# Kernel tuning notes

Measured on AMD Instinct MI355X. Metric: run time of the kernel, lower is better.

The kernel has to match this reference:

```python
import jax, jax.numpy as jnp
import numpy as np

N, E, G, H, NF, EF, GF, L = 204800, 600000, 3200, 128, 16, 5, 8, 6
EPS = 1e-5


def setup_inputs() -> dict:
    key = jax.random.key(0)
    ks = jax.random.split(key, 24)
    s = 0.05
    inp = {
        'x': jax.random.normal(ks[0], (N, NF), jnp.float32),
        'edge_index': jax.random.randint(ks[1], (2, E), 0, N, jnp.int32),
        'edge_attr': jax.random.normal(ks[2], (E, EF), jnp.float32),
        'global_features': jax.random.normal(ks[3], (G, GF), jnp.float32),
        'batch': (jnp.arange(N, dtype=jnp.int32) // (N // G)),
        'node_w': jax.random.normal(ks[4], (NF, H), jnp.float32) * s,
        'node_b': jnp.zeros((H,), jnp.float32),
        'edge_w': jax.random.normal(ks[5], (EF, H), jnp.float32) * s,
        'edge_b': jnp.zeros((H,), jnp.float32),
        'rel_w': jax.random.normal(ks[6], (L, H, H), jnp.float32) * s,
        'rel_b': jnp.zeros((L, H), jnp.float32),
        'root_w': jax.random.normal(ks[7], (L, H, H), jnp.float32) * s,
        'bn_gamma': jnp.ones((L, H), jnp.float32),
        'bn_beta': jnp.zeros((L, H), jnp.float32),
        'gate_w1': jax.random.normal(ks[8], (H, H), jnp.float32) * s,
        'gate_b1': jnp.zeros((H,), jnp.float32),
        'gate_w2': jax.random.normal(ks[9], (H, 1), jnp.float32) * s,
        'gate_b2': jnp.zeros((1,), jnp.float32),
        'gf_w': jax.random.normal(ks[10], (GF, H), jnp.float32) * s,
        'gf_b': jnp.zeros((H,), jnp.float32),
        'gi_w': jax.random.normal(ks[11], (2 * H, H), jnp.float32) * s,
        'gi_b': jnp.zeros((H,), jnp.float32),
    }
    return inp


def reference(x, edge_index, edge_attr, global_features, batch,
              node_w, node_b, edge_w, edge_b,
              rel_w, rel_b, root_w, bn_gamma, bn_beta,
              gate_w1, gate_b1, gate_w2, gate_b2,
              gf_w, gf_b, gi_w, gi_b):
    n = x.shape[0]
    src, dst = edge_index[0], edge_index[1]
    h = x @ node_w + node_b                       # [N,H]
    ea = edge_attr @ edge_w + edge_b              # [E,H]
    for i in range(L):
        identity = h
        msg = h[src] * ea                         # [E,H] gather + edge weighting
        agg = jax.ops.segment_sum(msg, dst, num_segments=n)  # scatter-add
        h2 = agg @ rel_w[i] + rel_b[i] + h @ root_w[i]        # GraphConv
        mean = jnp.mean(h2, axis=0)
        var = jnp.mean(jnp.square(h2 - mean), axis=0)         # biased (BN train)
        h2 = (h2 - mean) * jax.lax.rsqrt(var + EPS) * bn_gamma[i] + bn_beta[i]
        h = jax.nn.relu(h2 + identity)
    # GlobalAttention: segment softmax over gate scores, weighted sum of h
    gate = (jax.nn.relu(h @ gate_w1 + gate_b1) @ gate_w2 + gate_b2)[:, 0]  # [N]
    m = jax.ops.segment_max(gate, batch, num_segments=G)
    e = jnp.exp(gate - m[batch])
    ssum = jax.ops.segment_sum(e, batch, num_segments=G)
    alpha = e / ssum[batch]
    pooled = jax.ops.segment_sum(alpha[:, None] * h, batch, num_segments=G)  # [G,H]
    gf = global_features @ gf_w + gf_b
    global_embedding = jnp.concatenate([pooled, gf], axis=1) @ gi_w + gi_b
    return (h, global_embedding)
```

## Files before the change

### kernel.cpp

```cpp
#include <hip/hip_runtime.h>
#include <math.h>

#define N_NODES 204800
#define N_EDGES 600000
#define N_GRAPH 3200
#define H 128
#define NF 16
#define EF 5
#define GF 8
#define LAYERS 6
#define SEG 64
#define EPSV 1e-5f
#define NB_SCAN 800
#define NBLK 3200

typedef __attribute__((ext_vector_type(8))) short bf16x8;
typedef __attribute__((ext_vector_type(4))) float f32x4;

__device__ inline float bf2f(unsigned int u) {
    return __builtin_bit_cast(float, u << 16);
}
__device__ inline unsigned short f2bf(float f) {
    unsigned int u = __builtin_bit_cast(unsigned int, f);
    u += 0x7fffu + ((u >> 16) & 1u);
    return (unsigned short)(u >> 16);
}
__device__ inline float uif(unsigned int u) { return __builtin_bit_cast(float, u); }

__global__ __launch_bounds__(64) void k_wpack_init(
    const float* __restrict__ nw, unsigned short* __restrict__ nwp)
{
    int nb = blockIdx.x;
    int l = threadIdx.x;
    int col = nb * 16 + (l & 15);
    int kb = (l >> 4) * 8;
    unsigned short tmp[8];
#pragma unroll
    for (int m = 0; m < 8; ++m) {
        int k = kb + m;
        tmp[m] = (k < NF) ? f2bf(nw[(size_t)k * H + col]) : (unsigned short)0;
    }
    *(uint4*)(nwp + ((size_t)nb * 64 + l) * 8) = *(uint4*)tmp;
}

__global__ __launch_bounds__(256) void k_init_mfma(
    const float* __restrict__ x, const unsigned short* __restrict__ nwp,
    const float* __restrict__ node_b, unsigned short* __restrict__ hb)
{
    __shared__ unsigned short xt[64][40];
    int tid = threadIdx.x;
    int w = tid >> 6, l = tid & 63;
    int n0 = blockIdx.x * 64;
    int lr = l & 15, hi = l >> 4;

    int row = tid >> 2, q = tid & 3;
    float4 xv = *(const float4*)(x + (size_t)(n0 + row) * NF + q * 4);
    xt[row][q * 4 + 0] = f2bf(xv.x);
    xt[row][q * 4 + 1] = f2bf(xv.y);
    xt[row][q * 4 + 2] = f2bf(xv.z);
    xt[row][q * 4 + 3] = f2bf(xv.w);
    *(uint2*)&xt[row][16 + q * 4] = make_uint2(0, 0);
    __syncthreads();

    f32x4 acc[4][2];
#pragma unroll
    for (int rb = 0; rb < 4; ++rb) {
        acc[rb][0] = (f32x4){0.f, 0.f, 0.f, 0.f};
        acc[rb][1] = (f32x4){0.f, 0.f, 0.f, 0.f};
    }
    const bf16x8* wv = (const bf16x8*)nwp;
    bf16x8 b0 = wv[(2 * w + 0) * 64 + l];
    bf16x8 b1 = wv[(2 * w + 1) * 64 + l];
#pragma unroll
    for (int rb = 0; rb < 4; ++rb) {
        bf16x8 a = *(const bf16x8*)&xt[rb * 16 + lr][hi * 8];
        acc[rb][0] = __builtin_amdgcn_mfma_f32_16x16x32_bf16(a, b0, acc[rb][0], 0, 0, 0);
        acc[rb][1] = __builtin_amdgcn_mfma_f32_16x16x32_bf16(a, b1, acc[rb][1], 0, 0, 0);
    }

#pragma unroll
    for (int nbl = 0; nbl < 2; ++nbl) {
        int col = w * 32 + nbl * 16 + lr;
        float bs = node_b[col];
#pragma unroll
        for (int rb = 0; rb < 4; ++rb)
#pragma unroll
            for (int jj = 0; jj < 4; ++jj)
                hb[(size_t)(n0 + rb * 16 + hi * 4 + jj) * H + col] = f2bf(acc[rb][nbl][jj] + bs);
    }
}

__global__ __launch_bounds__(64) void k_wpack(
    const float* __restrict__ relw, const float* __restrict__ rootw,
    unsigned short* __restrict__ wp)
{
    int bid = blockIdx.x;
    int i = bid >> 6, f = bid & 63;
    int nb = f >> 3, ks = f & 7;
    int l = threadIdx.x;
    const float* src = (ks < 4) ? (relw + (size_t)i * H * H) : (rootw + (size_t)i * H * H);
    int ksl = ks & 3;
    int col = nb * 16 + (l & 15);
    int kbase = ksl * 32 + (l >> 4) * 8;
    unsigned short tmp[8];
#pragma unroll
    for (int m = 0; m < 8; ++m)
        tmp[m] = f2bf(src[(size_t)(kbase + m) * H + col]);
    *(uint4*)(wp + ((size_t)bid * 64 + l) * 8) = *(uint4*)tmp;
}

__global__ __launch_bounds__(64) void k_wpack_gate(
    const float* __restrict__ gw1, unsigned short* __restrict__ gwp)
{
    int bid = blockIdx.x;
    int nb = bid >> 2, ks = bid & 3;
    int l = threadIdx.x;
    int col = nb * 16 + (l & 15);
    int kbase = ks * 32 + (l >> 4) * 8;
    unsigned short tmp[8];
#pragma unroll
    for (int m = 0; m < 8; ++m)
        tmp[m] = f2bf(gw1[(size_t)(kbase + m) * H + col]);
    *(uint4*)(gwp + ((size_t)bid * 64 + l) * 8) = *(uint4*)tmp;
}

__global__ __launch_bounds__(256) void k_deg(const int* __restrict__ ei, int* __restrict__ deg)
{
    int e = blockIdx.x * 256 + threadIdx.x;
    if (e < N_EDGES) atomicAdd(&deg[ei[N_EDGES + e]], 1);
}

__global__ __launch_bounds__(256) void k_scan1(
    const int* __restrict__ deg, int* __restrict__ rowtmp, int* __restrict__ bsum)
{
    __shared__ int sh[256];
    int t = threadIdx.x;
    int i = blockIdx.x * 256 + t;
    int v = deg[i];
    sh[t] = v;
    __syncthreads();
    for (int off = 1; off < 256; off <<= 1) {
        int a = (t >= off) ? sh[t - off] : 0;
        __syncthreads();
        sh[t] += a;
        __syncthreads();
    }
    rowtmp[i] = sh[t] - v;
    if (t == 255) bsum[blockIdx.x] = sh[255];
}

__global__ void k_scan2(int* __restrict__ bsum, int* __restrict__ boff)
{
    __shared__ int sh[256];
    __shared__ int carry;
    int t = threadIdx.x;
    if (t == 0) carry = 0;
    __syncthreads();
    for (int base = 0; base < NB_SCAN; base += 256) {
        int i = base + t;
        int v = (i < NB_SCAN) ? bsum[i] : 0;
        sh[t] = v;
        __syncthreads();
        for (int off = 1; off < 256; off <<= 1) {
            int a = (t >= off) ? sh[t - off] : 0;
            __syncthreads();
            sh[t] += a;
            __syncthreads();
        }
        if (i < NB_SCAN) boff[i] = carry + sh[t] - v;
        __syncthreads();
        if (t == 0) carry += sh[255];
        __syncthreads();
    }
}

__global__ __launch_bounds__(256) void k_scan3(
    const int* __restrict__ rowtmp, const int* __restrict__ boff,
    int* __restrict__ rowptr, int* __restrict__ cursor)
{
    int i = blockIdx.x * 256 + threadIdx.x;
    int r = rowtmp[i] + boff[blockIdx.x];
    rowptr[i] = r;
    cursor[i] = r;
    if (i == 0) rowptr[N_NODES] = N_EDGES;
}

__global__ __launch_bounds__(256) void k_scatter(
    const int* __restrict__ ei, const float* __restrict__ eattr,
    int* __restrict__ cursor, uint4* __restrict__ recs)
{
    int e = blockIdx.x * 256 + threadIdx.x;
    if (e >= N_EDGES) return;
    int d = ei[N_EDGES + e];
    const float* ar = eattr + (size_t)e * EF;
    float c0 = ar[0], c1 = ar[1], c2 = ar[2], c3 = ar[3], c4 = ar[4];
    int pos = atomicAdd(&cursor[d], 1);
    uint4 q0, q1;
    q0.x = (unsigned int)ei[e];
    q0.y = __builtin_bit_cast(unsigned int, c0);
    q0.z = __builtin_bit_cast(unsigned int, c1);
    q0.w = __builtin_bit_cast(unsigned int, c2);
    q1.x = __builtin_bit_cast(unsigned int, c3);
    q1.y = __builtin_bit_cast(unsigned int, c4);
    q1.z = 0; q1.w = 0;
    recs[2 * (size_t)pos]     = q0;
    recs[2 * (size_t)pos + 1] = q1;
}

#define FOLD(jj, q0, q1, hv)                                                   \
    if ((jj) < jend) {                                                         \
        while ((jj) >= nend) {                                                 \
            *(unsigned int*)(aggb + (size_t)(n0 + cur) * H + 2 * l) =          \
                (unsigned int)f2bf(a0) | ((unsigned int)f2bf(a1) << 16);       \
            a0 = 0.f; a1 = 0.f; ++cur; nend = __shfl(rpv, cur + 1);            \
        }                                                                      \
        float ea0 = eb2.x, ea1 = eb2.y;                                        \
        float c0 = uif((q0).y), c1 = uif((q0).z), c2 = uif((q0).w);            \
        float c3 = uif((q1).x), c4 = uif((q1).y);                              \
        ea0 += c0 * ew2[0].x + c1 * ew2[1].x + c2 * ew2[2].x + c3 * ew2[3].x + c4 * ew2[4].x; \
        ea1 += c0 * ew2[0].y + c1 * ew2[1].y + c2 * ew2[2].y + c3 * ew2[3].y + c4 * ew2[4].y; \
        a0 += bf2f((hv) & 0xffffu) * ea0;                                      \
        a1 += bf2f((hv) >> 16) * ea1;                                          \
    }

__global__ __launch_bounds__(256) void k_agg(
    const int* __restrict__ rowptr, const uint4* __restrict__ recs,
    const float* __restrict__ edge_w, const float* __restrict__ edge_b,
    const unsigned short* __restrict__ hb, unsigned short* __restrict__ aggb)
{
    int w = threadIdx.x >> 6, l = threadIdx.x & 63;
    int n0 = (blockIdx.x * 4 + w) * 8;
    float2 ew2[EF];
#pragma unroll
    for (int k = 0; k < EF; ++k) ew2[k] = ((const float2*)(edge_w + k * H))[l];
    float2 eb2 = ((const float2*)edge_b)[l];

    int rpv = rowptr[n0 + (l < 9 ? l : 8)];
    int jbeg = __shfl(rpv, 0), jend = __shfl(rpv, 8);
    int cur = 0;
    int nend = __shfl(rpv, 1);
    float a0 = 0.f, a1 = 0.f;

    for (int j = jbeg; j < jend; j += 4) {
        int jc1 = min(j + 1, jend - 1);
        int jc2 = min(j + 2, jend - 1);
        int jc3 = min(j + 3, jend - 1);
        uint4 qa0 = recs[2 * (size_t)j],   qa1 = recs[2 * (size_t)j + 1];
        uint4 qb0 = recs[2 * (size_t)jc1], qb1 = recs[2 * (size_t)jc1 + 1];
        uint4 qc0 = recs[2 * (size_t)jc2], qc1 = recs[2 * (size_t)jc2 + 1];
        uint4 qd0 = recs[2 * (size_t)jc3], qd1 = recs[2 * (size_t)jc3 + 1];
        unsigned int hva = *(const unsigned int*)(hb + (size_t)(int)qa0.x * H + 2 * l);
        unsigned int hvb = *(const unsigned int*)(hb + (size_t)(int)qb0.x * H + 2 * l);
        unsigned int hvc = *(const unsigned int*)(hb + (size_t)(int)qc0.x * H + 2 * l);
        unsigned int hvd = *(const unsigned int*)(hb + (size_t)(int)qd0.x * H + 2 * l);
        FOLD(j,     qa0, qa1, hva);
        FOLD(j + 1, qb0, qb1, hvb);
        FOLD(j + 2, qc0, qc1, hvc);
        FOLD(j + 3, qd0, qd1, hvd);
    }
    while (cur < 8) {
        *(unsigned int*)(aggb + (size_t)(n0 + cur) * H + 2 * l) =
            (unsigned int)f2bf(a0) | ((unsigned int)f2bf(a1) << 16);
        a0 = 0.f; a1 = 0.f; ++cur;
    }
}

__global__ __launch_bounds__(256) void k_gemm_mfma(
    const unsigned short* __restrict__ aggb,
    const unsigned short* __restrict__ hb,
    const unsigned short* __restrict__ wp,
    const float* __restrict__ relb,
    unsigned short* __restrict__ h2b,
    float* __restrict__ pbuf)
{
    __shared__ unsigned short smA[64 * 128];
    __shared__ unsigned short smH[64 * 128];
    int tid = threadIdx.x;
    int w = tid >> 6, l = tid & 63;
    int bid = blockIdx.x;
    int n0 = bid * 64;
    int lr = l & 15, hi = l >> 4;

    const char* aggp = (const char*)(aggb + (size_t)n0 * H);
    const char* hbp  = (const char*)(hb  + (size_t)n0 * H);
    char* sA = (char*)smA;
    char* sH = (char*)smH;
#pragma unroll
    for (int i = 0; i < 4; ++i) {
        int o = (i * 256 + tid) * 16;
        int row = o >> 8;
        int col = o & 255;
        int scol = col ^ ((row & 7) << 4);
        uint4 va = *(const uint4*)(aggp + o);
        uint4 vh = *(const uint4*)(hbp + o);
        *(uint4*)(sA + row * 256 + scol) = va;
        *(uint4*)(sH + row * 256 + scol) = vh;
    }
    __syncthreads();

    f32x4 acc[4][2];
#pragma unroll
    for (int rb = 0; rb < 4; ++rb) {
        acc[rb][0] = (f32x4){0.f, 0.f, 0.f, 0.f};
        acc[rb][1] = (f32x4){0.f, 0.f, 0.f, 0.f};
    }

    const bf16x8* wv = (const bf16x8*)wp;
#pragma unroll
    for (int ks = 0; ks < 4; ++ks) {
        bf16x8 b0 = wv[((2 * w + 0) * 8 + ks) * 64 + l];
        bf16x8 b1 = wv[((2 * w + 1) * 8 + ks) * 64 + l];
#pragma unroll
        for (int rb = 0; rb < 4; ++rb) {
            int r = rb * 16 + lr;
            int bc = (ks * 64 + hi * 16) ^ ((r & 7) << 4);
            bf16x8 a = *(const bf16x8*)(sA + r * 256 + bc);
            acc[rb][0] = __builtin_amdgcn_mfma_f32_16x16x32_bf16(a, b0, acc[rb][0], 0, 0, 0);
            acc[rb][1] = __builtin_amdgcn_mfma_f32_16x16x32_bf16(a, b1, acc[rb][1], 0, 0, 0);
        }
    }
#pragma unroll
    for (int ks = 0; ks < 4; ++ks) {
        bf16x8 b0 = wv[((2 * w + 0) * 8 + 4 + ks) * 64 + l];
        bf16x8 b1 = wv[((2 * w + 1) * 8 + 4 + ks) * 64 + l];
#pragma unroll
        for (int rb = 0; rb < 4; ++rb) {
            int r = rb * 16 + lr;
            int bc = (ks * 64 + hi * 16) ^ ((r & 7) << 4);
            bf16x8 a = *(const bf16x8*)(sH + r * 256 + bc);
            acc[rb][0] = __builtin_amdgcn_mfma_f32_16x16x32_bf16(a, b0, acc[rb][0], 0, 0, 0);
            acc[rb][1] = __builtin_amdgcn_mfma_f32_16x16x32_bf16(a, b1, acc[rb][1], 0, 0, 0);
        }
    }

#pragma unroll
    for (int nbl = 0; nbl < 2; ++nbl) {
        int col = w * 32 + nbl * 16 + lr;
        float bs = relb[col];
        float csum = 0.f, csq = 0.f;
#pragma unroll
        for (int rb = 0; rb < 4; ++rb) {
#pragma unroll
            for (int jj = 0; jj < 4; ++jj) {
                float v = acc[rb][nbl][jj] + bs;
                h2b[(size_t)(n0 + rb * 16 + hi * 4 + jj) * H + col] = f2bf(v);
                csum += v; csq += v * v;
            }
        }
        csum += __shfl_xor(csum, 16); csum += __shfl_xor(csum, 32);
        csq  += __shfl_xor(csq, 16);  csq  += __shfl_xor(csq, 32);
        if (hi == 0) {
            pbuf[(size_t)col * NBLK + bid]         = csum;
            pbuf[(size_t)(128 + col) * NBLK + bid] = csq;
        }
    }
}

__global__ __launch_bounds__(256) void k_red(
    const float* __restrict__ pbuf, const float* __restrict__ gamma,
    const float* __restrict__ beta, float* __restrict__ stats)
{
    __shared__ float sh[8];
    int c = blockIdx.x;
    int t = threadIdx.x;
    float s = 0.f, q = 0.f;
    const float* ps = pbuf + (size_t)c * NBLK;
    const float* pq = pbuf + (size_t)(128 + c) * NBLK;
    for (int i = t; i < NBLK; i += 256) { s += ps[i]; q += pq[i]; }
#pragma unroll
    for (int off = 32; off >= 1; off >>= 1) {
        s += __shfl_xor(s, off);
        q += __shfl_xor(q, off);
    }
    if ((t & 63) == 0) { sh[t >> 6] = s; sh[4 + (t >> 6)] = q; }
    __syncthreads();
    if (t == 0) {
        float S = sh[0] + sh[1] + sh[2] + sh[3];
        float Q = sh[4] + sh[5] + sh[6] + sh[7];
        float mean = S / (float)N_NODES;
        float var = fmaxf(Q / (float)N_NODES - mean * mean, 0.f);
        float scale = gamma[c] * rsqrtf(var + EPSV);
        stats[c] = scale;
        stats[128 + c] = beta[c] - mean * scale;
    }
}

template<bool LAST>
__global__ __launch_bounds__(256) void k_bn_apply(
    const unsigned short* __restrict__ h2b, const float* __restrict__ stats,
    unsigned short* __restrict__ hb, float* __restrict__ h)
{
    __shared__ float ssc[H], ssh[H];
    int tid = threadIdx.x;
    if (tid < H) {
        ssc[tid] = stats[tid];
        ssh[tid] = stats[128 + tid];
    }
    __syncthreads();
    size_t base = ((size_t)blockIdx.x * 256 + tid) * 8;
    int c = (int)(base & 127);
    uint4 hv2 = *(const uint4*)(h2b + base);
    uint4 hvp = *(const uint4*)(hb + base);
    unsigned int u2[4] = {hv2.x, hv2.y, hv2.z, hv2.w};
    unsigned int up[4] = {hvp.x, hvp.y, hvp.z, hvp.w};
    float o[8];
#pragma unroll
    for (int k = 0; k < 4; ++k) {
        float vlo = bf2f(u2[k] & 0xffffu), vhi = bf2f(u2[k] >> 16);
        float plo = bf2f(up[k] & 0xffffu), phi = bf2f(up[k] >> 16);
        o[2 * k]     = fmaxf(vlo * ssc[c + 2 * k]     + ssh[c + 2 * k]     + plo, 0.f);
        o[2 * k + 1] = fmaxf(vhi * ssc[c + 2 * k + 1] + ssh[c + 2 * k + 1] + phi, 0.f);
    }
    uint4 pk;
    pk.x = (unsigned int)f2bf(o[0]) | ((unsigned int)f2bf(o[1]) << 16);
    pk.y = (unsigned int)f2bf(o[2]) | ((unsigned int)f2bf(o[3]) << 16);
    pk.z = (unsigned int)f2bf(o[4]) | ((unsigned int)f2bf(o[5]) << 16);
    pk.w = (unsigned int)f2bf(o[6]) | ((unsigned int)f2bf(o[7]) << 16);
    *(uint4*)(hb + base) = pk;
    if (LAST) {
        *(float4*)(h + base)     = make_float4(o[0], o[1], o[2], o[3]);
        *(float4*)(h + base + 4) = make_float4(o[4], o[5], o[6], o[7]);
    }
}

__global__ __launch_bounds__(256) void k_gate_pool(
    const unsigned short* __restrict__ hb,
    const unsigned short* __restrict__ gwp,
    const float* __restrict__ b1, const float* __restrict__ w2,
    const float* __restrict__ b2, float* __restrict__ pooled)
{
    __shared__ float Red[512];
    __shared__ float al[64];
    int tid = threadIdx.x;
    int w = tid >> 6, l = tid & 63;
    int lr = l & 15, hi = l >> 4;
    int g = blockIdx.x;
    int n0 = g * SEG;

    f32x4 acc[4][2];
#pragma unroll
    for (int rb = 0; rb < 4; ++rb) {
        acc[rb][0] = (f32x4){0.f, 0.f, 0.f, 0.f};
        acc[rb][1] = (f32x4){0.f, 0.f, 0.f, 0.f};
    }
    const bf16x8* wv = (const bf16x8*)gwp;
#pragma unroll
    for (int ks = 0; ks < 4; ++ks) {
        bf16x8 bb0 = wv[((2 * w + 0) * 4 + ks) * 64 + l];
        bf16x8 bb1 = wv[((2 * w + 1) * 4 + ks) * 64 + l];
#pragma unroll
        for (int rb = 0; rb < 4; ++rb) {
            bf16x8 a = *(const bf16x8*)(hb + (size_t)(n0 + rb * 16 + lr) * H + ks * 32 + hi * 8);
            acc[rb][0] = __builtin_amdgcn_mfma_f32_16x16x32_bf16(a, bb0, acc[rb][0], 0, 0, 0);
            acc[rb][1] = __builtin_amdgcn_mfma_f32_16x16x32_bf16(a, bb1, acc[rb][1], 0, 0, 0);
        }
    }
    int col0 = w * 32 + lr, col1 = w * 32 + 16 + lr;
    float b10 = b1[col0], b11 = b1[col1];
    float w20 = w2[col0], w21 = w2[col1];
    float p[4][4];
#pragma unroll
    for (int rb = 0; rb < 4; ++rb)
#pragma unroll
        for (int jj = 0; jj < 4; ++jj) {
            float v0 = fmaxf(acc[rb][0][jj] + b10, 0.f);
            float v1 = fmaxf(acc[rb][1][jj] + b11, 0.f);
            float s = v0 * w20 + v1 * w21;
            s += __shfl_xor(s, 1); s += __shfl_xor(s, 2);
            s += __shfl_xor(s, 4); s += __shfl_xor(s, 8);
            p[rb][jj] = s;
        }
    if (lr == 0) {
#pragma unroll
        for (int rb = 0; rb < 4; ++rb)
#pragma unroll
            for (int jj = 0; jj < 4; ++jj)
                Red[w * 64 + rb * 16 + hi * 4 + jj] = p[rb][jj];
    }
    __syncthreads();
    if (tid < 64) {
        float gt = Red[tid] + Red[64 + tid] + Red[128 + tid] + Red[192 + tid] + b2[0];
        float m = gt;
#pragma unroll
        for (int off = 32; off >= 1; off >>= 1) m = fmaxf(m, __shfl_xor(m, off));
        float e = expf(gt - m);
        float s = e;
#pragma unroll
        for (int off = 32; off >= 1; off >>= 1) s += __shfl_xor(s, off);
        al[tid] = e / s;
    }
    __syncthreads();
    int cq = tid & 63, qd = tid >> 6;
    float p0 = 0.f, p1 = 0.f;
    const unsigned short* hbase = hb + (size_t)n0 * H;
    for (int j = qd * 16; j < qd * 16 + 16; ++j) {
        unsigned int hv = *(const unsigned int*)(hbase + (size_t)j * H + 2 * cq);
        float a = al[j];
        p0 += a * bf2f(hv & 0xffffu);
        p1 += a * bf2f(hv >> 16);
    }
    Red[qd * 128 + 2 * cq]     = p0;
    Red[qd * 128 + 2 * cq + 1] = p1;
    __syncthreads();
    if (tid < 128)
        pooled[(size_t)g * H + tid] = Red[tid] + Red[128 + tid] + Red[256 + tid] + Red[384 + tid];
}

__global__ __launch_bounds__(128) void k_final(
    const float* __restrict__ pooled, const float* __restrict__ gfeat,
    const float* __restrict__ gf_w, const float* __restrict__ gf_b,
    const float* __restrict__ gi_w, const float* __restrict__ gi_b,
    float* __restrict__ out)
{
    int g = blockIdx.x, c = threadIdx.x;
    __shared__ float prow[H], gfs[H];
    prow[c] = pooled[(size_t)g * H + c];
    float gv = gf_b[c];
    const float* gr = gfeat + (size_t)g * GF;
#pragma unroll
    for (int k = 0; k < GF; ++k) gv += gr[k] * gf_w[k * H + c];
    gfs[c] = gv;
    __syncthreads();
    float acc = gi_b[c];
    for (int k = 0; k < H; ++k) acc += prow[k] * gi_w[k * H + c];
    for (int k = 0; k < H; ++k) acc += gfs[k] * gi_w[(H + k) * H + c];
    out[(size_t)N_NODES * H + (size_t)g * H + c] = acc;
}

extern "C" void kernel_launch(void* const* d_in, const int* in_sizes, int n_in,
                              void* d_out, int out_size, void* d_ws, size_t ws_size,
                              hipStream_t stream)
{
    const float* x       = (const float*)d_in[0];
    const int*   ei      = (const int*)d_in[1];
    const float* eattr   = (const float*)d_in[2];
    const float* gfeat   = (const float*)d_in[3];
    const float* node_w  = (const float*)d_in[5];
    const float* node_b  = (const float*)d_in[6];
    const float* edge_w  = (const float*)d_in[7];
    const float* edge_b  = (const float*)d_in[8];
    const float* rel_w   = (const float*)d_in[9];
    const float* rel_b   = (const float*)d_in[10];
    const float* root_w  = (const float*)d_in[11];
    const float* bn_g    = (const float*)d_in[12];
    const float* bn_b    = (const float*)d_in[13];
    const float* gate_w1 = (const float*)d_in[14];
    const float* gate_b1 = (const float*)d_in[15];
    const float* gate_w2 = (const float*)d_in[16];
    const float* gate_b2 = (const float*)d_in[17];
    const float* gf_w    = (const float*)d_in[18];
    const float* gf_b    = (const float*)d_in[19];
    const float* gi_w    = (const float*)d_in[20];
    const float* gi_b    = (const float*)d_in[21];

    float* h   = (float*)d_out;
    float* out = (float*)d_out;

    char* wsb = (char*)d_ws;
    size_t off = 0;
    auto take = [&](size_t bytes) -> char* {
        char* r = wsb + off;
        off = (off + bytes + 63) & ~(size_t)63;
        return r;
    };
    unsigned short* h2b  = (unsigned short*)take((size_t)N_NODES * H * 2);
    unsigned short* hb   = (unsigned short*)take((size_t)N_NODES * H * 2);
    unsigned short* aggb = (unsigned short*)take((size_t)N_NODES * H * 2);
    unsigned short* wpck = (unsigned short*)take((size_t)LAYERS * 32768 * 2);
    unsigned short* gwp  = (unsigned short*)take((size_t)16384 * 2);
    unsigned short* nwp  = (unsigned short*)take((size_t)4096 * 2);
    float* pbuf   = (float*)take((size_t)256 * NBLK * 4);
    float* stats  = (float*)take((size_t)256 * 4);
    float* pooled = (float*)take((size_t)N_GRAPH * H * 4);
    int*   deg    = (int*)take((size_t)N_NODES * 4);
    int*   rowptr = (int*)take((size_t)(N_NODES + 1) * 4);
    int*   cursor = (int*)take((size_t)N_NODES * 4);
    int*   bsum   = (int*)take((size_t)NB_SCAN * 4);
    int*   boff   = (int*)take((size_t)NB_SCAN * 4);
    uint4* recs   = (uint4*)take((size_t)N_EDGES * 32);
    int*   rowtmp = cursor;

    hipMemsetAsync(deg, 0, N_NODES * sizeof(int), stream);
    k_deg<<<(N_EDGES + 255) / 256, 256, 0, stream>>>(ei, deg);
    k_scan1<<<NB_SCAN, 256, 0, stream>>>(deg, rowtmp, bsum);
    k_scan2<<<1, 256, 0, stream>>>(bsum, boff);
    k_scan3<<<NB_SCAN, 256, 0, stream>>>(rowtmp, boff, rowptr, cursor);
    k_scatter<<<(N_EDGES + 255) / 256, 256, 0, stream>>>(ei, eattr, cursor, recs);
    k_wpack<<<LAYERS * 64, 64, 0, stream>>>(rel_w, root_w, wpck);
    k_wpack_gate<<<32, 64, 0, stream>>>(gate_w1, gwp);
    k_wpack_init<<<8, 64, 0, stream>>>(node_w, nwp);

    k_init_mfma<<<NBLK, 256, 0, stream>>>(x, nwp, node_b, hb);

    for (int i = 0; i < LAYERS; ++i) {
        k_agg<<<N_NODES / 32, 256, 0, stream>>>(rowptr, recs, edge_w, edge_b, hb, aggb);
        k_gemm_mfma<<<NBLK, 256, 0, stream>>>(
            aggb, hb, wpck + (size_t)i * 32768, rel_b + (size_t)i * H,
            h2b, pbuf);
        k_red<<<128, 256, 0, stream>>>(pbuf, bn_g + (size_t)i * H, bn_b + (size_t)i * H, stats);
        if (i < LAYERS - 1)
            k_bn_apply<false><<<N_NODES * H / 8 / 256, 256, 0, stream>>>(h2b, stats, hb, h);
        else
            k_bn_apply<true><<<N_NODES * H / 8 / 256, 256, 0, stream>>>(h2b, stats, hb, h);
    }

    k_gate_pool<<<N_GRAPH, 256, 0, stream>>>(hb, gwp, gate_b1, gate_w2, gate_b2, pooled);
    k_final<<<N_GRAPH, H, 0, stream>>>(pooled, gfeat, gf_w, gf_b, gi_w, gi_b, out);
}
```

Measured before the change: 933.0 us.

## Precompute edge embeddings once in CSR order as bf16 instead of per-layer recompute

Adds a kernel that computes the edge_attr projection once per edge, rounds it to bf16, and stores it at the edge's CSR position. The aggregation kernel then reads this per-edge 128-wide vector and a compact source index instead of recomputing the 5-term projection from packed records each layer. This removes per-layer FMA work but greatly increases memory traffic: each layer now streams a 128-channel bf16 row per edge rather than a 32-byte record. It also rounds edge embeddings to bf16.

```diff
diff --git a/kernel.cpp b/kernel.cpp
--- a/kernel.cpp
+++ b/kernel.cpp
@@ -186,55 +186,51 @@
 }
 
 __global__ __launch_bounds__(256) void k_scatter(
-    const int* __restrict__ ei, const float* __restrict__ eattr,
-    int* __restrict__ cursor, uint4* __restrict__ recs)
+    const int* __restrict__ ei, int* __restrict__ cursor,
+    int* __restrict__ srcs, int* __restrict__ posArr)
 {
     int e = blockIdx.x * 256 + threadIdx.x;
     if (e >= N_EDGES) return;
     int d = ei[N_EDGES + e];
+    int pos = atomicAdd(&cursor[d], 1);
+    srcs[pos] = ei[e];
+    posArr[e] = pos;
+}
+
+__global__ __launch_bounds__(256) void k_ea(
+    const float* __restrict__ eattr, const int* __restrict__ posArr,
+    const float* __restrict__ edge_w, const float* __restrict__ edge_b,
+    unsigned short* __restrict__ eab)
+{
+    int t = threadIdx.x;
+    int e = blockIdx.x * 2 + (t >> 7);
+    int c = t & 127;
+    int pos = posArr[e];
     const float* ar = eattr + (size_t)e * EF;
-    float c0 = ar[0], c1 = ar[1], c2 = ar[2], c3 = ar[3], c4 = ar[4];
-    int pos = atomicAdd(&cursor[d], 1);
-    uint4 q0, q1;
-    q0.x = (unsigned int)ei[e];
-    q0.y = __builtin_bit_cast(unsigned int, c0);
-    q0.z = __builtin_bit_cast(unsigned int, c1);
-    q0.w = __builtin_bit_cast(unsigned int, c2);
-    q1.x = __builtin_bit_cast(unsigned int, c3);
-    q1.y = __builtin_bit_cast(unsigned int, c4);
-    q1.z = 0; q1.w = 0;
-    recs[2 * (size_t)pos]     = q0;
-    recs[2 * (size_t)pos + 1] = q1;
-}
-
-#define FOLD(jj, q0, q1, hv)                                                   \
+    float ea = edge_b[c];
+#pragma unroll
+    for (int k = 0; k < EF; ++k) ea += ar[k] * edge_w[k * H + c];
+    eab[(size_t)pos * H + c] = f2bf(ea);
+}
+
+#define FOLD(jj, ev, hv)                                                       \
     if ((jj) < jend) {                                                         \
         while ((jj) >= nend) {                                                 \
             *(unsigned int*)(aggb + (size_t)(n0 + cur) * H + 2 * l) =          \
                 (unsigned int)f2bf(a0) | ((unsigned int)f2bf(a1) << 16);       \
             a0 = 0.f; a1 = 0.f; ++cur; nend = __shfl(rpv, cur + 1);            \
         }                                                                      \
-        float ea0 = eb2.x, ea1 = eb2.y;                                        \
-        float c0 = uif((q0).y), c1 = uif((q0).z), c2 = uif((q0).w);            \
-        float c3 = uif((q1).x), c4 = uif((q1).y);                              \
-        ea0 += c0 * ew2[0].x + c1 * ew2[1].x + c2 * ew2[2].x + c3 * ew2[3].x + c4 * ew2[4].x; \
-        ea1 += c0 * ew2[0].y + c1 * ew2[1].y + c2 * ew2[2].y + c3 * ew2[3].y + c4 * ew2[4].y; \
-        a0 += bf2f((hv) & 0xffffu) * ea0;                                      \
-        a1 += bf2f((hv) >> 16) * ea1;                                          \
+        a0 += bf2f((hv) & 0xffffu) * bf2f((ev) & 0xffffu);                     \
+        a1 += bf2f((hv) >> 16) * bf2f((ev) >> 16);                             \
     }
 
 __global__ __launch_bounds__(256) void k_agg(
-    const int* __restrict__ rowptr, const uint4* __restrict__ recs,
-    const float* __restrict__ edge_w, const float* __restrict__ edge_b,
+    const int* __restrict__ rowptr, const int* __restrict__ srcs,
+    const unsigned short* __restrict__ eab,
     const unsigned short* __restrict__ hb, unsigned short* __restrict__ aggb)
 {
     int w = threadIdx.x >> 6, l = threadIdx.x & 63;
     int n0 = (blockIdx.x * 4 + w) * 8;
-    float2 ew2[EF];
-#pragma unroll
-    for (int k = 0; k < EF; ++k) ew2[k] = ((const float2*)(edge_w + k * H))[l];
-    float2 eb2 = ((const float2*)edge_b)[l];
-
     int rpv = rowptr[n0 + (l < 9 ? l : 8)];
     int jbeg = __shfl(rpv, 0), jend = __shfl(rpv, 8);
     int cur = 0;
@@ -245,18 +241,19 @@
         int jc1 = min(j + 1, jend - 1);
         int jc2 = min(j + 2, jend - 1);
         int jc3 = min(j + 3, jend - 1);
-        uint4 qa0 = recs[2 * (size_t)j],   qa1 = recs[2 * (size_t)j + 1];
-        uint4 qb0 = recs[2 * (size_t)jc1], qb1 = recs[2 * (size_t)jc1 + 1];
-        uint4 qc0 = recs[2 * (size_t)jc2], qc1 = recs[2 * (size_t)jc2 + 1];
-        uint4 qd0 = recs[2 * (size_t)jc3], qd1 = recs[2 * (size_t)jc3 + 1];
-        unsigned int hva = *(const unsigned int*)(hb + (size_t)(int)qa0.x * H + 2 * l);
-        unsigned int hvb = *(const unsigned int*)(hb + (size_t)(int)qb0.x * H + 2 * l);
-        unsigned int hvc = *(const unsigned int*)(hb + (size_t)(int)qc0.x * H + 2 * l);
-        unsigned int hvd = *(const unsigned int*)(hb + (size_t)(int)qd0.x * H + 2 * l);
-        FOLD(j,     qa0, qa1, hva);
-        FOLD(j + 1, qb0, qb1, hvb);
-        FOLD(j + 2, qc0, qc1, hvc);
-        FOLD(j + 3, qd0, qd1, hvd);
+        int s0 = srcs[j], s1 = srcs[jc1], s2 = srcs[jc2], s3 = srcs[jc3];
+        unsigned int ev0 = *(const unsigned int*)(eab + (size_t)j   * H + 2 * l);
+        unsigned int ev1 = *(const unsigned int*)(eab + (size_t)jc1 * H + 2 * l);
+        unsigned int ev2 = *(const unsigned int*)(eab + (size_t)jc2 * H + 2 * l);
+        unsigned int ev3 = *(const unsigned int*)(eab + (size_t)jc3 * H + 2 * l);
+        unsigned int hv0 = *(const unsigned int*)(hb + (size_t)s0 * H + 2 * l);
+        unsigned int hv1 = *(const unsigned int*)(hb + (size_t)s1 * H + 2 * l);
+        unsigned int hv2 = *(const unsigned int*)(hb + (size_t)s2 * H + 2 * l);
+        unsigned int hv3 = *(const unsigned int*)(hb + (size_t)s3 * H + 2 * l);
+        FOLD(j,     ev0, hv0);
+        FOLD(j + 1, ev1, hv1);
+        FOLD(j + 2, ev2, hv2);
+        FOLD(j + 3, ev3, hv3);
     }
     while (cur < 8) {
         *(unsigned int*)(aggb + (size_t)(n0 + cur) * H + 2 * l) =
@@ -577,7 +574,9 @@
     int*   cursor = (int*)take((size_t)N_NODES * 4);
     int*   bsum   = (int*)take((size_t)NB_SCAN * 4);
     int*   boff   = (int*)take((size_t)NB_SCAN * 4);
-    uint4* recs   = (uint4*)take((size_t)N_EDGES * 32);
+    int*   srcs   = (int*)take((size_t)N_EDGES * 4);
+    int*   posArr = (int*)take((size_t)N_EDGES * 4);
+    unsigned short* eab = (unsigned short*)take((size_t)N_EDGES * H * 2);
     int*   rowtmp = cursor;
 
     hipMemsetAsync(deg, 0, N_NODES * sizeof(int), stream);
@@ -585,7 +584,8 @@
     k_scan1<<<NB_SCAN, 256, 0, stream>>>(deg, rowtmp, bsum);
     k_scan2<<<1, 256, 0, stream>>>(bsum, boff);
     k_scan3<<<NB_SCAN, 256, 0, stream>>>(rowtmp, boff, rowptr, cursor);
-    k_scatter<<<(N_EDGES + 255) / 256, 256, 0, stream>>>(ei, eattr, cursor, recs);
+    k_scatter<<<(N_EDGES + 255) / 256, 256, 0, stream>>>(ei, cursor, srcs, posArr);
+    k_ea<<<N_EDGES / 2, 256, 0, stream>>>(eattr, posArr, edge_w, edge_b, eab);
     k_wpack<<<LAYERS * 64, 64, 0, stream>>>(rel_w, root_w, wpck);
     k_wpack_gate<<<32, 64, 0, stream>>>(gate_w1, gwp);
     k_wpack_init<<<8, 64, 0, stream>>>(node_w, nwp);
@@ -593,7 +593,7 @@
     k_init_mfma<<<NBLK, 256, 0, stream>>>(x, nwp, node_b, hb);
 
     for (int i = 0; i < LAYERS; ++i) {
-        k_agg<<<N_NODES / 32, 256, 0, stream>>>(rowptr, recs, edge_w, edge_b, hb, aggb);
+        k_agg<<<N_NODES / 32, 256, 0, stream>>>(rowptr, srcs, eab, hb, aggb);
         k_gemm_mfma<<<NBLK, 256, 0, stream>>>(
             aggb, hb, wpck + (size_t)i * 32768, rel_b + (size_t)i * H,
             h2b, pbuf);
```

Result: slower. 1.113 ms (+19.3%).
